# Optimization experiments

Hardware: AMD Instinct MI355X
Metric: run time of the kernel (lower is better)

## Reference

```python
import jax, jax.numpy as jnp
import numpy as np

B, C_IN, N = 128, 256, 1024
C_OUT = 256
L = 3069  # 3 * (N - 1) triplet indices, multiple of kernel_size=3


def setup_inputs() -> dict:
    key = jax.random.key(0)
    k1, k2, k3, k4 = jax.random.split(key, 4)
    data = jax.random.normal(k1, (B, C_IN, N), dtype=jnp.float32)
    indexes = jax.random.randint(k2, (B, L, 1), 0, N, dtype=jnp.int64)
    # Conv1d(in_dims, out_dims, kernel_size=3) params, PyTorch layout [out, in, k]
    fan_in = C_IN * 3
    bound = 1.0 / np.sqrt(fan_in)
    weight = jax.random.uniform(k3, (C_OUT, C_IN, 3), dtype=jnp.float32, minval=-bound, maxval=bound)
    bias = jax.random.uniform(k4, (C_OUT,), dtype=jnp.float32, minval=-bound, maxval=bound)
    return {"data": data, "indexes": indexes, "weight": weight, "bias": bias}


def reference(data, indexes, weight, bias):
    # gather: data[b, c, indexes[b, l, 0]] -> [B, C_IN, L]
    idx = indexes[:, :, 0]  # [B, L]
    gathered = jnp.take_along_axis(data, idx[:, None, :], axis=2)  # broadcast over channel dim
    # Conv1d kernel_size=3 stride=3 == per-triplet matmul:
    # reshape [B, C_IN, L] -> [B, C_IN, L//3, 3]; contract with weight [C_OUT, C_IN, 3]
    trip = gathered.reshape(B, gathered.shape[1], L // 3, 3)
    feats = jnp.einsum('bcnk,ock->bon', trip, weight) + bias[None, :, None]  # [B, C_OUT, L//3]
    # prepend a zero column (padding slot for node index 0)
    zeros = jnp.zeros((feats.shape[0], feats.shape[1], 1), dtype=feats.dtype)
    feats = jnp.concatenate((zeros, feats), axis=2)  # [B, C_OUT, L//3 + 1]
    return (feats, indexes)
```

## Files before the change

kernel.cpp:

```cpp
#include <hip/hip_runtime.h>

#define B_      128
#define C_IN_   256
#define NPTS    1024
#define C_OUT_  256
#define L_      3069
#define NTRIP   1023
#define T_OUT   1024
#define FEATS_SIZE (B_ * C_OUT_ * T_OUT)
#define KTOT    768

#define BK      96
#define NCHUNK  8
#define THREADS 512

typedef __attribute__((ext_vector_type(8))) short           bf16x8;
typedef __attribute__((ext_vector_type(8))) unsigned short  ushort8;
typedef __attribute__((ext_vector_type(4))) unsigned short  ushort4v;
typedef __attribute__((ext_vector_type(4))) float           f32x4;

__device__ __forceinline__ unsigned short f2bf(float f) {
    union { float f; unsigned u; } v; v.f = f;
    unsigned r = (v.u + 0x7FFFu + ((v.u >> 16) & 1u)) >> 16;
    return (unsigned short)r;
}

__device__ __forceinline__ void gload16(const void* g, void* l) {
    __builtin_amdgcn_global_load_lds(
        (const __attribute__((address_space(1))) unsigned int*)g,
        (__attribute__((address_space(3))) unsigned int*)l, 16, 0, 0);
}

#define WOFF_T  0
#define DOFF_T  393216
#define WS_NEED_T2 (393216 + 67108864)

#define AS2     0
#define BS2     49152
#define SMEM2   81920
#define BN2     128

__global__ __launch_bounds__(256) void convert_w2(
    const float* __restrict__ w, unsigned short* __restrict__ wbf2)
{
    int i = blockIdx.x * 256 + threadIdx.x;
    if (i >= C_OUT_ * KTOT) return;
    int r  = i / KTOT;
    int g  = i - r * KTOT;
    int kc = g / BK;
    int e  = g - kc * BK;
    int tap = e >> 5;
    int lc  = e & 31;
    int korig = (kc * 32 + lc) * 3 + tap;
    unsigned short v = f2bf(w[r * KTOT + korig]);
    int addr = (r * 192 + e * 2) ^ ((r & 7) << 4);
    wbf2[(kc * 49152 + addr) >> 1] = v;
}

__global__ __launch_bounds__(256) void transpose_data(
    const float* __restrict__ data, unsigned short* __restrict__ dataT)
{
    __shared__ float T[64][68];
    const int bid = blockIdx.x;
    const int b   = bid >> 6;
    const int ct  = (bid & 63) >> 4;
    const int nt  = bid & 15;
    const int c0  = ct * 64, n0 = nt * 64;
    const int t   = threadIdx.x;
    const int row = t >> 2;
    const int q   = t & 3;

    const float* src = data + ((size_t)(b * C_IN_ + c0 + row)) * NPTS + n0 + q * 16;
    #pragma unroll
    for (int j = 0; j < 4; ++j) {
        float4 v = *(const float4*)(src + j * 4);
        *(float4*)&T[row][q * 16 + j * 4] = v;
    }
    __syncthreads();

    ushort8 o0, o1;
    #pragma unroll
    for (int j = 0; j < 8; ++j)  o0[j] = f2bf(T[q * 16 + j][row]);
    #pragma unroll
    for (int j = 0; j < 8; ++j)  o1[j] = f2bf(T[q * 16 + 8 + j][row]);
    unsigned short* dst = dataT + ((size_t)(b * NPTS) + n0 + row) * C_IN_ + c0 + q * 16;
    *(ushort8*)(dst)     = o0;
    *(ushort8*)(dst + 8) = o1;
}

__global__ __launch_bounds__(THREADS, 4) void treeconv_mfma2(
    const unsigned short* __restrict__ wbf2,
    const unsigned short* __restrict__ dataT,
    const int*   __restrict__ indexes,
    const float* __restrict__ bias,
    float*       __restrict__ out)
{
    __shared__ alignas(16) unsigned char smem[SMEM2];
    int* idx_s = (int*)(smem + BS2);

    const int tid = threadIdx.x;
    const int b   = blockIdx.x >> 3;
    const int nt0 = (blockIdx.x & 7) * BN2;

    if (tid < BN2 * 3) {
        int off = nt0 * 3 + tid;
        idx_s[tid] = (off < L_) ? indexes[b * L_ + off] : 0;
    }
    __syncthreads();

    const int lane = tid & 63;
    const int wid  = tid >> 6;
    const int wm   = wid >> 1;
    const int wn   = wid & 1;
    const int l15  = lane & 15;
    const int lg   = lane >> 4;

    unsigned boff[4];
    #pragma unroll
    for (int j = 0; j < 4; ++j) {
        int slot = wid * 256 + j * 64 + lane;
        int n    = slot >> 4;
        int el   = (slot & 15) ^ (n & 7);
        int tap  = (el < 12) ? (el >> 2) : 0;
        int q    = el & 3;
        int ix   = idx_s[n * 3 + tap];
        boff[j]  = (unsigned)(ix * (C_IN_ * 2) + q * 16);
    }
    __syncthreads();

    const char* dTb = (const char*)dataT + (size_t)b * NPTS * C_IN_ * 2;
    const char* wsrc = (const char*)wbf2;

    f32x4 acc[4][4];
    #pragma unroll
    for (int mi = 0; mi < 4; ++mi)
        #pragma unroll
        for (int ni = 0; ni < 4; ++ni)
            acc[mi][ni] = (f32x4){0.f, 0.f, 0.f, 0.f};

    for (int kc = 0; kc < NCHUNK; ++kc) {
        #pragma unroll
        for (int j = 0; j < 4; ++j) {
            gload16(dTb + (size_t)kc * 64 + boff[j],
                    smem + BS2 + wid * 4096 + j * 1024);
        }
        #pragma unroll
        for (int i = 0; i < 6; ++i) {
            int off = wid * 6144 + i * 1024;
            gload16(wsrc + (size_t)kc * 49152 + off + lane * 16,
                    smem + AS2 + off);
        }
        __syncthreads();

        #pragma unroll
        for (int ks = 0; ks < 3; ++ks) {
            const int kb = ks * 64 + lg * 16;
            bf16x8 bb[4];
            #pragma unroll
            for (int ni = 0; ni < 4; ++ni) {
                int row = wn * 64 + ni * 16 + l15;
                bb[ni] = *(const bf16x8*)(smem + BS2 + row * 256 + (kb ^ ((row & 7) << 4)));
            }
            #pragma unroll
            for (int mi = 0; mi < 4; ++mi) {
                int row = wm * 64 + mi * 16 + l15;
                bf16x8 av = *(const bf16x8*)(smem + ((row * 192 + kb) ^ ((row & 7) << 4)));
                #pragma unroll
                for (int ni = 0; ni < 4; ++ni)
                    acc[mi][ni] = __builtin_amdgcn_mfma_f32_16x16x32_bf16(
                        av, bb[ni], acc[mi][ni], 0, 0, 0);
            }
        }
        __syncthreads();
    }

    float* outB = out + (size_t)b * (C_OUT_ * T_OUT);
    #pragma unroll
    for (int mi = 0; mi < 4; ++mi) {
        #pragma unroll
        for (int r = 0; r < 4; ++r) {
            int o = wm * 64 + mi * 16 + lg * 4 + r;
            float bv = bias[o];
            #pragma unroll
            for (int ni = 0; ni < 4; ++ni) {
                int n = nt0 + wn * 64 + ni * 16 + l15;
                if (n < NTRIP)
                    outB[o * T_OUT + 1 + n] = acc[mi][ni][r] + bv;
            }
        }
    }
}

#define BN      64
#define AS_OFF  0
#define BS_OFF  49152
#define IDX_OFF 61440
#define SMEM_BYTES 62208

template<bool PREW>
__global__ __launch_bounds__(THREADS, 4) void treeconv_mfma(
    const float* __restrict__ data,
    const int*   __restrict__ indexes,
    const float* __restrict__ w32,
    const unsigned short* __restrict__ wbf,
    const float* __restrict__ bias,
    float*       __restrict__ out)
{
    __shared__ alignas(16) unsigned char smem[SMEM_BYTES];
    int* idx_s = (int*)(smem + IDX_OFF);

    const int tid = threadIdx.x;
    const int b   = blockIdx.x >> 4;
    const int nt0 = (blockIdx.x & 15) * BN;

    if (tid < BN * 3) {
        int off = nt0 * 3 + tid;
        idx_s[tid] = (off < L_) ? indexes[b * L_ + off] : 0;
    }
    __syncthreads();

    const int lane = tid & 63;
    const int wid  = tid >> 6;
    const int wm   = wid >> 1;
    const int wn   = wid & 1;
    const int l15  = lane & 15;
    const int lg   = lane >> 4;

    f32x4 acc[4][2];
    #pragma unroll
    for (int mi = 0; mi < 4; ++mi)
        #pragma unroll
        for (int ni = 0; ni < 2; ++ni)
            acc[mi][ni] = (f32x4){0.f, 0.f, 0.f, 0.f};

    const float* dataB = data + (size_t)b * (C_IN_ * NPTS);
    const int ar = tid >> 1;
    const int ah = tid & 1;
    const int gn = tid & 63;
    const int g8 = tid >> 6;

    for (int kc = 0; kc < NCHUNK; ++kc) {
        {
            const int ab = ar * 192 + ah * 96;
            const int sw = (ar & 7) << 4;
            if (PREW) {
                const ushort8* src = (const ushort8*)(wbf + ar * KTOT + kc * BK + ah * 48);
                #pragma unroll
                for (int j = 0; j < 6; ++j) {
                    ushort8 v = src[j];
                    *(ushort8*)(smem + ((ab + j * 16) ^ sw)) = v;
                }
            } else {
                const float* src = w32 + ar * KTOT + kc * BK + ah * 48;
                #pragma unroll
                for (int j = 0; j < 6; ++j) {
                    float4 fa = *(const float4*)(src + j * 8);
                    float4 fb = *(const float4*)(src + j * 8 + 4);
                    ushort8 v;
                    v[0] = f2bf(fa.x); v[1] = f2bf(fa.y); v[2] = f2bf(fa.z); v[3] = f2bf(fa.w);
                    v[4] = f2bf(fb.x); v[5] = f2bf(fb.y); v[6] = f2bf(fb.z); v[7] = f2bf(fb.w);
                    *(ushort8*)(smem + ((ab + j * 16) ^ sw)) = v;
                }
            }
        }
        {
            const int* ip = idx_s + gn * 3;
            int ix0 = ip[0], ix1 = ip[1], ix2 = ip[2];
            const float* dp = dataB + (kc * 32 + g8 * 4) * NPTS;
            unsigned short vals[12];
            #pragma unroll
            for (int ci = 0; ci < 4; ++ci) {
                vals[ci * 3 + 0] = f2bf(dp[ix0]);
                vals[ci * 3 + 1] = f2bf(dp[ix1]);
                vals[ci * 3 + 2] = f2bf(dp[ix2]);
                dp += NPTS;
            }
            const int bb = BS_OFF + gn * 192 + g8 * 24;
            const int sw = (gn & 7) << 4;
            #pragma unroll
            for (int q = 0; q < 3; ++q) {
                ushort4v v;
                v[0] = vals[q * 4 + 0]; v[1] = vals[q * 4 + 1];
                v[2] = vals[q * 4 + 2]; v[3] = vals[q * 4 + 3];
                *(ushort4v*)(smem + ((bb + q * 8) ^ sw)) = v;
            }
        }
        __syncthreads();

        #pragma unroll
        for (int ks = 0; ks < 3; ++ks) {
            bf16x8 a[4], bf[2];
            const int kb = ks * 64 + lg * 16;
            #pragma unroll
            for (int mi = 0; mi < 4; ++mi) {
                int row = wm * 64 + mi * 16 + l15;
                a[mi] = *(const bf16x8*)(smem + ((row * 192 + kb) ^ ((row & 7) << 4)));
            }
            #pragma unroll
            for (int ni = 0; ni < 2; ++ni) {
                int row = wn * 32 + ni * 16 + l15;
                bf[ni] = *(const bf16x8*)(smem + ((BS_OFF + row * 192 + kb) ^ ((row & 7) << 4)));
            }
            #pragma unroll
            for (int mi = 0; mi < 4; ++mi)
                #pragma unroll
                for (int ni = 0; ni < 2; ++ni)
                    acc[mi][ni] = __builtin_amdgcn_mfma_f32_16x16x32_bf16(
                        a[mi], bf[ni], acc[mi][ni], 0, 0, 0);
        }
        __syncthreads();
    }

    float* outB = out + (size_t)b * (C_OUT_ * T_OUT);
    #pragma unroll
    for (int mi = 0; mi < 4; ++mi) {
        #pragma unroll
        for (int r = 0; r < 4; ++r) {
            int o = wm * 64 + mi * 16 + lg * 4 + r;
            float bv = bias[o];
            #pragma unroll
            for (int ni = 0; ni < 2; ++ni) {
                int n = nt0 + wn * 32 + ni * 16 + l15;
                if (n < NTRIP)
                    outB[o * T_OUT + 1 + n] = acc[mi][ni][r] + bv;
            }
        }
    }
}

__global__ __launch_bounds__(256) void convert_w(
    const float* __restrict__ w, unsigned short* __restrict__ wbf)
{
    int i = (blockIdx.x * 256 + threadIdx.x) * 4;
    if (i < C_OUT_ * KTOT) {
        float4 f = *(const float4*)(w + i);
        ushort4v v;
        v[0] = f2bf(f.x); v[1] = f2bf(f.y); v[2] = f2bf(f.z); v[3] = f2bf(f.w);
        *(ushort4v*)(wbf + i) = v;
    }
}

__global__ __launch_bounds__(256) void aux_kernel(
    const int* __restrict__ indexes, float* __restrict__ out)
{
    int i = blockIdx.x * 256 + threadIdx.x;
    if (i < B_ * L_)
        out[FEATS_SIZE + i] = (float)indexes[i];
    if (i < B_ * C_OUT_)
        out[(size_t)i * T_OUT] = 0.0f;
}

extern "C" void kernel_launch(void* const* d_in, const int* in_sizes, int n_in,
                              void* d_out, int out_size, void* d_ws, size_t ws_size,
                              hipStream_t stream)
{
    const float* data    = (const float*)d_in[0];
    const int*   indexes = (const int*)d_in[1];
    const float* weight  = (const float*)d_in[2];
    const float* bias    = (const float*)d_in[3];
    float* out = (float*)d_out;

    hipLaunchKernelGGL(aux_kernel, dim3((B_ * L_ + 255) / 256), dim3(256), 0, stream,
                       indexes, out);

    if (ws_size >= (size_t)WS_NEED_T2) {
        unsigned short* wbf2  = (unsigned short*)((char*)d_ws + WOFF_T);
        unsigned short* dataT = (unsigned short*)((char*)d_ws + DOFF_T);
        hipLaunchKernelGGL(convert_w2, dim3((C_OUT_ * KTOT + 255) / 256), dim3(256),
                           0, stream, weight, wbf2);
        hipLaunchKernelGGL(transpose_data, dim3(B_ * 64), dim3(256), 0, stream,
                           data, dataT);
        hipLaunchKernelGGL(treeconv_mfma2, dim3(B_ * 8), dim3(THREADS), 0, stream,
                           wbf2, dataT, indexes, bias, out);
    } else if (ws_size >= (size_t)(C_OUT_ * KTOT * 2)) {
        unsigned short* wbf = (unsigned short*)d_ws;
        hipLaunchKernelGGL(convert_w, dim3((C_OUT_ * KTOT / 4 + 255) / 256), dim3(256),
                           0, stream, weight, wbf);
        hipLaunchKernelGGL((treeconv_mfma<true>), dim3(B_ * 16), dim3(THREADS), 0, stream,
                           data, indexes, weight, wbf, bias, out);
    } else {
        hipLaunchKernelGGL((treeconv_mfma<false>), dim3(B_ * 16), dim3(THREADS), 0, stream,
                           data, indexes, weight, (const unsigned short*)d_ws, bias, out);
    }
}
```

Before: 133.1 us.

## Load weights directly from global in MFMA fragment order and register-prefetch gathered data

Pre-permutes the bf16 weights into the exact per-lane MFMA A-fragment order so each wave reads them straight from global (L2-resident) memory instead of staging them in LDS. The gathered data tile now goes through registers with a one-chunk-ahead software prefetch and is written into LDS, replacing the direct global-to-LDS async loads. LDS use drops from 80 KB to about 34 KB, which may let more blocks fit per CU. The cost is repeated global/L2 traffic for weights, since each wave in a block refetches them. It also adds register pressure for the prefetch buffer and an extra barrier per chunk.

```diff
diff --git a/kernel.cpp b/kernel.cpp
--- a/kernel.cpp
+++ b/kernel.cpp
@@ -25,36 +25,27 @@
     return (unsigned short)r;
 }
 
-__device__ __forceinline__ void gload16(const void* g, void* l) {
-    __builtin_amdgcn_global_load_lds(
-        (const __attribute__((address_space(1))) unsigned int*)g,
-        (__attribute__((address_space(3))) unsigned int*)l, 16, 0, 0);
-}
-
 #define WOFF_T  0
 #define DOFF_T  393216
 #define WS_NEED_T2 (393216 + 67108864)
 
-#define AS2     0
-#define BS2     49152
-#define SMEM2   81920
+#define IDX3    32768
+#define SMEM3   34304
 #define BN2     128
 
-__global__ __launch_bounds__(256) void convert_w2(
-    const float* __restrict__ w, unsigned short* __restrict__ wbf2)
+__global__ __launch_bounds__(256) void convert_w3(
+    const float* __restrict__ w, unsigned short* __restrict__ wbf3)
 {
     int i = blockIdx.x * 256 + threadIdx.x;
     if (i >= C_OUT_ * KTOT) return;
-    int r  = i / KTOT;
-    int g  = i - r * KTOT;
-    int kc = g / BK;
-    int e  = g - kc * BK;
-    int tap = e >> 5;
-    int lc  = e & 31;
-    int korig = (kc * 32 + lc) * 3 + tap;
-    unsigned short v = f2bf(w[r * KTOT + korig]);
-    int addr = (r * 192 + e * 2) ^ ((r & 7) << 4);
-    wbf2[(kc * 49152 + addr) >> 1] = v;
+    int j   = i & 7;
+    int lgv = (i >> 3) & 3;
+    int row = (i >> 5) & 255;
+    int c   = i >> 13;
+    int ks  = c % 3;
+    int kc  = c / 3;
+    int korig = (kc * 32 + lgv * 8 + j) * 3 + ks;
+    wbf3[i] = f2bf(w[row * KTOT + korig]);
 }
 
 __global__ __launch_bounds__(256) void transpose_data(
@@ -88,15 +79,15 @@
     *(ushort8*)(dst + 8) = o1;
 }
 
-__global__ __launch_bounds__(THREADS, 4) void treeconv_mfma2(
-    const unsigned short* __restrict__ wbf2,
+__global__ __launch_bounds__(THREADS, 4) void treeconv_mfma3(
+    const unsigned short* __restrict__ wbf3,
     const unsigned short* __restrict__ dataT,
     const int*   __restrict__ indexes,
     const float* __restrict__ bias,
     float*       __restrict__ out)
 {
-    __shared__ alignas(16) unsigned char smem[SMEM2];
-    int* idx_s = (int*)(smem + BS2);
+    __shared__ alignas(16) unsigned char smem[SMEM3];
+    int* idx_s = (int*)(smem + IDX3);
 
     const int tid = threadIdx.x;
     const int b   = blockIdx.x >> 3;
@@ -126,10 +117,11 @@
         int ix   = idx_s[n * 3 + tap];
         boff[j]  = (unsigned)(ix * (C_IN_ * 2) + q * 16);
     }
-    __syncthreads();
-
-    const char* dTb = (const char*)dataT + (size_t)b * NPTS * C_IN_ * 2;
-    const char* wsrc = (const char*)wbf2;
+
+    const char* dTb  = (const char*)dataT + (size_t)b * NPTS * C_IN_ * 2;
+    const char* wsrc = (const char*)wbf3;
+    const int   aoff = wm * 4096 + l15 * 64 + lg * 16;
+    unsigned char* bdst = smem + wid * 4096 + lane * 16;
 
     f32x4 acc[4][4];
     #pragma unroll
@@ -138,40 +130,45 @@
         for (int ni = 0; ni < 4; ++ni)
             acc[mi][ni] = (f32x4){0.f, 0.f, 0.f, 0.f};
 
+    f32x4 breg[4];
+    #pragma unroll
+    for (int j = 0; j < 4; ++j)
+        breg[j] = *(const f32x4*)(dTb + boff[j]);
+
     for (int kc = 0; kc < NCHUNK; ++kc) {
-        #pragma unroll
-        for (int j = 0; j < 4; ++j) {
-            gload16(dTb + (size_t)kc * 64 + boff[j],
-                    smem + BS2 + wid * 4096 + j * 1024);
-        }
-        #pragma unroll
-        for (int i = 0; i < 6; ++i) {
-            int off = wid * 6144 + i * 1024;
-            gload16(wsrc + (size_t)kc * 49152 + off + lane * 16,
-                    smem + AS2 + off);
-        }
         __syncthreads();
-
+        #pragma unroll
+        for (int j = 0; j < 4; ++j)
+            *(f32x4*)(bdst + j * 1024) = breg[j];
+        __syncthreads();
+
+        if (kc + 1 < NCHUNK) {
+            #pragma unroll
+            for (int j = 0; j < 4; ++j)
+                breg[j] = *(const f32x4*)(dTb + (kc + 1) * 64 + boff[j]);
+        }
+
+        const char* wchunk = wsrc + kc * 49152;
         #pragma unroll
         for (int ks = 0; ks < 3; ++ks) {
+            bf16x8 a[4];
+            #pragma unroll
+            for (int mi = 0; mi < 4; ++mi)
+                a[mi] = *(const bf16x8*)(wchunk + ks * 16384 + mi * 1024 + aoff);
             const int kb = ks * 64 + lg * 16;
             bf16x8 bb[4];
             #pragma unroll
             for (int ni = 0; ni < 4; ++ni) {
                 int row = wn * 64 + ni * 16 + l15;
-                bb[ni] = *(const bf16x8*)(smem + BS2 + row * 256 + (kb ^ ((row & 7) << 4)));
-            }
-            #pragma unroll
-            for (int mi = 0; mi < 4; ++mi) {
-                int row = wm * 64 + mi * 16 + l15;
-                bf16x8 av = *(const bf16x8*)(smem + ((row * 192 + kb) ^ ((row & 7) << 4)));
+                bb[ni] = *(const bf16x8*)(smem + row * 256 + (kb ^ ((row & 7) << 4)));
+            }
+            #pragma unroll
+            for (int mi = 0; mi < 4; ++mi)
                 #pragma unroll
                 for (int ni = 0; ni < 4; ++ni)
                     acc[mi][ni] = __builtin_amdgcn_mfma_f32_16x16x32_bf16(
-                        av, bb[ni], acc[mi][ni], 0, 0, 0);
-            }
-        }
-        __syncthreads();
+                        a[mi], bb[ni], acc[mi][ni], 0, 0, 0);
+        }
     }
 
     float* outB = out + (size_t)b * (C_OUT_ * T_OUT);
@@ -364,14 +361,14 @@
                        indexes, out);
 
     if (ws_size >= (size_t)WS_NEED_T2) {
-        unsigned short* wbf2  = (unsigned short*)((char*)d_ws + WOFF_T);
+        unsigned short* wbf3  = (unsigned short*)((char*)d_ws + WOFF_T);
         unsigned short* dataT = (unsigned short*)((char*)d_ws + DOFF_T);
-        hipLaunchKernelGGL(convert_w2, dim3((C_OUT_ * KTOT + 255) / 256), dim3(256),
-                           0, stream, weight, wbf2);
+        hipLaunchKernelGGL(convert_w3, dim3((C_OUT_ * KTOT + 255) / 256), dim3(256),
+                           0, stream, weight, wbf3);
         hipLaunchKernelGGL(transpose_data, dim3(B_ * 64), dim3(256), 0, stream,
                            data, dataT);
-        hipLaunchKernelGGL(treeconv_mfma2, dim3(B_ * 8), dim3(THREADS), 0, stream,
-                           wbf2, dataT, indexes, bias, out);
+        hipLaunchKernelGGL(treeconv_mfma3, dim3(B_ * 8), dim3(THREADS), 0, stream,
+                           wbf3, dataT, indexes, bias, out);
     } else if (ws_size >= (size_t)(C_OUT_ * KTOT * 2)) {
         unsigned short* wbf = (unsigned short*)d_ws;
         hipLaunchKernelGGL(convert_w, dim3((C_OUT_ * KTOT / 4 + 255) / 256), dim3(256),
```

After: 143.8 us. +8.0%, slower.
